# Optimization experiments

Hardware: AMD Instinct MI355X
Metric: run time of the kernel (lower is better)

The kernel has to match this reference:

```python
import jax, jax.numpy as jnp
import numpy as np

B, T, C, HS = 1024, 256, 384, 64

def setup_inputs() -> dict:
    key = jax.random.key(0)
    kx, kq, kk, kv = jax.random.split(key, 4)
    x = jax.random.normal(kx, (B, T, C), dtype=jnp.float32)
    # torch Linear(no bias): y = x @ W.T with W [hs, C]; store transposed [C, hs]
    s = 1.0 / np.sqrt(C)
    Wq = jax.random.uniform(kq, (C, HS), jnp.float32, -s, s)
    Wk = jax.random.uniform(kk, (C, HS), jnp.float32, -s, s)
    Wv = jax.random.uniform(kv, (C, HS), jnp.float32, -s, s)
    return {"x": x, "Wq": Wq, "Wk": Wk, "Wv": Wv}

def reference(x, Wq, Wk, Wv):
    Tn = x.shape[1]
    hs = Wq.shape[1]
    q = x @ Wq  # [B,T,hs]
    k = x @ Wk
    v = x @ Wv
    scores = jnp.einsum('bqd,bkd->bqk', q, k) * (hs ** -0.5)  # [B,T,T]
    causal = jnp.tril(jnp.ones((Tn, Tn), dtype=bool))
    scores = jnp.where(causal[None, :, :], scores, -jnp.inf)
    wei = jax.nn.softmax(scores, axis=-1)
    out = jnp.einsum('bqk,bkd->bqd', wei, v)  # [B,T,hs]
    return out
```

## Files before the change

### kernel.cpp

```cpp
#include <hip/hip_runtime.h>
#include <hip/hip_bf16.h>

#define TT 256
#define CC 384
#define HSZ 64

typedef __attribute__((ext_vector_type(8))) short bf16x8;
typedef __attribute__((ext_vector_type(4))) float f32x4;

static __device__ __forceinline__ unsigned short f2bf(float f) {
    union { __hip_bfloat16 h; unsigned short u; } cv;
    cv.h = __float2bfloat16(f);
    return cv.u;
}

static __device__ __forceinline__ bf16x8 cvt8(float4 a, float4 b) {
    bf16x8 r;
    r[0] = (short)f2bf(a.x); r[1] = (short)f2bf(a.y);
    r[2] = (short)f2bf(a.z); r[3] = (short)f2bf(a.w);
    r[4] = (short)f2bf(b.x); r[5] = (short)f2bf(b.y);
    r[6] = (short)f2bf(b.z); r[7] = (short)f2bf(b.w);
    return r;
}

__global__ __launch_bounds__(256) void wtrans_kernel(
        const float* __restrict__ Wq,
        const float* __restrict__ Wk,
        const float* __restrict__ Wv,
        unsigned short* __restrict__ Wt) {
    int idx = blockIdx.x * 256 + threadIdx.x;
    if (idx >= 192 * CC) return;
    int n = idx / CC;
    int ck = idx - n * CC;
    const float* W = (n < 64) ? Wq : ((n < 128) ? Wk : Wv);
    Wt[n * CC + ck] = f2bf(W[ck * HSZ + (n & 63)]);
}

__global__ __launch_bounds__(256, 2) void qkv_kernel(
        const float* __restrict__ x,
        const unsigned short* __restrict__ Wt,
        unsigned short* __restrict__ qw,
        unsigned short* __restrict__ kw,
        unsigned short* __restrict__ vtw) {
    const int lane = threadIdx.x & 63;
    const int wv   = threadIdx.x >> 6;
    const int c    = lane & 15;
    const int quad = lane >> 4;
    const int rowbase = blockIdx.x * 128 + wv * 32;

    f32x4 acc[2][12];
    #pragma unroll
    for (int t = 0; t < 2; ++t)
        #pragma unroll
        for (int n = 0; n < 12; ++n)
            acc[t][n] = (f32x4){0.f, 0.f, 0.f, 0.f};

    const float* xa0 = x + (size_t)(rowbase + c) * CC + quad * 8;
    const float* xa1 = xa0 + 16 * CC;
    const unsigned short* wb = Wt + c * CC + quad * 8;

    for (int s = 0; s < 12; ++s) {
        float4 a0lo = *(const float4*)(xa0 + s * 32);
        float4 a0hi = *(const float4*)(xa0 + s * 32 + 4);
        float4 a1lo = *(const float4*)(xa1 + s * 32);
        float4 a1hi = *(const float4*)(xa1 + s * 32 + 4);
        bf16x8 a0 = cvt8(a0lo, a0hi);
        bf16x8 a1 = cvt8(a1lo, a1hi);
        #pragma unroll
        for (int n = 0; n < 12; ++n) {
            bf16x8 b = *(const bf16x8*)(wb + n * 16 * CC + s * 32);
            acc[0][n] = __builtin_amdgcn_mfma_f32_16x16x32_bf16(a0, b, acc[0][n], 0, 0, 0);
            acc[1][n] = __builtin_amdgcn_mfma_f32_16x16x32_bf16(a1, b, acc[1][n], 0, 0, 0);
        }
    }

    #pragma unroll
    for (int t = 0; t < 2; ++t) {
        const int mbase = rowbase + t * 16 + quad * 4;
        #pragma unroll
        for (int n = 0; n < 8; ++n) {
            unsigned short* dst = (n < 4) ? qw : kw;
            const int cg = (n & 3) * 16 + c;
            #pragma unroll
            for (int r = 0; r < 4; ++r)
                dst[(size_t)(mbase + r) * HSZ + cg] = f2bf(acc[t][n][r]);
        }
        const int bidx = mbase >> 8;
        const int tok  = mbase & 255;
        #pragma unroll
        for (int n = 8; n < 12; ++n) {
            const int hsg = (n - 8) * 16 + c;
            ushort4 pk;
            pk.x = f2bf(acc[t][n][0]);
            pk.y = f2bf(acc[t][n][1]);
            pk.z = f2bf(acc[t][n][2]);
            pk.w = f2bf(acc[t][n][3]);
            *(ushort4*)(vtw + (size_t)bidx * (HSZ * TT) + hsg * TT + tok) = pk;
        }
    }
}

__global__ __launch_bounds__(256, 2) void attn_kernel(
        const unsigned short* __restrict__ qw,
        const unsigned short* __restrict__ kw,
        const unsigned short* __restrict__ vtw,
        float* __restrict__ outp) {
    __shared__ __align__(16) unsigned short pbuf[4][16][40];
    const int b    = blockIdx.x;
    const int lane = threadIdx.x & 63;
    const int wv   = threadIdx.x >> 6;
    const int c    = lane & 15;
    const int quad = lane >> 4;

    const unsigned short* qb = qw  + (size_t)b * TT * HSZ;
    const unsigned short* kb = kw  + (size_t)b * TT * HSZ;
    const unsigned short* vb = vtw + (size_t)b * HSZ * TT;
    float*                ob = outp + (size_t)b * TT * HSZ;

    bf16x8 qf[4][2];
    #pragma unroll
    for (int i = 0; i < 4; ++i) {
        const int rb = (wv + 4 * i) * 16;
        #pragma unroll
        for (int ks = 0; ks < 2; ++ks)
            qf[i][ks] = *(const bf16x8*)(qb + (rb + c) * HSZ + ks * 32 + quad * 8);
    }

    f32x4 of[4][4];
    f32x4 mst[4], lst[4];
    #pragma unroll
    for (int i = 0; i < 4; ++i) {
        mst[i] = (f32x4){-1e30f, -1e30f, -1e30f, -1e30f};
        lst[i] = (f32x4){0.f, 0.f, 0.f, 0.f};
        #pragma unroll
        for (int n = 0; n < 4; ++n)
            of[i][n] = (f32x4){0.f, 0.f, 0.f, 0.f};
    }

    const float qscale = 0.18033688011112042f;

    for (int kt = 0; kt < 8; ++kt) {
        const int k0 = kt * 32;
        bf16x8 kf[2][2], vf[4];
        #pragma unroll
        for (int nt = 0; nt < 2; ++nt)
            #pragma unroll
            for (int ks = 0; ks < 2; ++ks)
                kf[nt][ks] = *(const bf16x8*)(kb + (k0 + nt * 16 + c) * HSZ + ks * 32 + quad * 8);
        #pragma unroll
        for (int n = 0; n < 4; ++n)
            vf[n] = *(const bf16x8*)(vb + (n * 16 + c) * TT + k0 + quad * 8);

        #pragma unroll
        for (int i = 0; i < 4; ++i) {
            const int mt = wv + 4 * i;
            if (mt < 2 * kt) continue;
            const int rb = mt * 16;

            f32x4 s0 = {0.f, 0.f, 0.f, 0.f}, s1 = {0.f, 0.f, 0.f, 0.f};
            #pragma unroll
            for (int ks = 0; ks < 2; ++ks) {
                s0 = __builtin_amdgcn_mfma_f32_16x16x32_bf16(qf[i][ks], kf[0][ks], s0, 0, 0, 0);
                s1 = __builtin_amdgcn_mfma_f32_16x16x32_bf16(qf[i][ks], kf[1][ks], s1, 0, 0, 0);
            }

            f32x4 t0, t1;
            #pragma unroll
            for (int r = 0; r < 4; ++r) { t0[r] = s0[r] * qscale; t1[r] = s1[r] * qscale; }

            if (mt < 2 * kt + 2) {
                #pragma unroll
                for (int r = 0; r < 4; ++r) {
                    const int row = rb + quad * 4 + r;
                    if (k0 + c > row)      t0[r] = -1e30f;
                    if (k0 + 16 + c > row) t1[r] = -1e30f;
                }
            }

            f32x4 mx;
            #pragma unroll
            for (int r = 0; r < 4; ++r) mx[r] = fmaxf(t0[r], t1[r]);
            #pragma unroll
            for (int off = 1; off < 16; off <<= 1)
                #pragma unroll
                for (int r = 0; r < 4; ++r)
                    mx[r] = fmaxf(mx[r], __shfl_xor(mx[r], off, 64));

            f32x4 mnew, alpha, p0, p1, rs;
            #pragma unroll
            for (int r = 0; r < 4; ++r) {
                mnew[r]  = fmaxf(mst[i][r], mx[r]);
                alpha[r] = exp2f(mst[i][r] - mnew[r]);
                p0[r]    = exp2f(t0[r] - mnew[r]);
                p1[r]    = exp2f(t1[r] - mnew[r]);
                rs[r]    = p0[r] + p1[r];
                mst[i][r] = mnew[r];
            }
            #pragma unroll
            for (int off = 1; off < 16; off <<= 1)
                #pragma unroll
                for (int r = 0; r < 4; ++r)
                    rs[r] += __shfl_xor(rs[r], off, 64);
            #pragma unroll
            for (int r = 0; r < 4; ++r)
                lst[i][r] = lst[i][r] * alpha[r] + rs[r];

            #pragma unroll
            for (int n = 0; n < 4; ++n)
                #pragma unroll
                for (int r = 0; r < 4; ++r)
                    of[i][n][r] *= alpha[r];

            #pragma unroll
            for (int r = 0; r < 4; ++r) {
                pbuf[wv][quad * 4 + r][c]      = f2bf(p0[r]);
                pbuf[wv][quad * 4 + r][16 + c] = f2bf(p1[r]);
            }
            bf16x8 pf = *(const bf16x8*)(&pbuf[wv][c][quad * 8]);
            #pragma unroll
            for (int n = 0; n < 4; ++n)
                of[i][n] = __builtin_amdgcn_mfma_f32_16x16x32_bf16(pf, vf[n], of[i][n], 0, 0, 0);
        }
    }

    #pragma unroll
    for (int i = 0; i < 4; ++i) {
        const int rb = (wv + 4 * i) * 16;
        f32x4 inv;
        #pragma unroll
        for (int r = 0; r < 4; ++r) inv[r] = 1.f / lst[i][r];
        #pragma unroll
        for (int n = 0; n < 4; ++n)
            #pragma unroll
            for (int r = 0; r < 4; ++r)
                ob[(size_t)(rb + quad * 4 + r) * HSZ + n * 16 + c] = of[i][n][r] * inv[r];
    }
}

extern "C" void kernel_launch(void* const* d_in, const int* in_sizes, int n_in,
                              void* d_out, int out_size, void* d_ws, size_t ws_size,
                              hipStream_t stream) {
    const float* x  = (const float*)d_in[0];
    const float* Wq = (const float*)d_in[1];
    const float* Wk = (const float*)d_in[2];
    const float* Wv = (const float*)d_in[3];
    float* outp = (float*)d_out;

    const int Bn = in_sizes[0] / (TT * CC);
    const size_t QKV_BYTES = (size_t)Bn * TT * HSZ * 2;

    char* ws = (char*)d_ws;
    unsigned short* Wt  = (unsigned short*)ws;
    unsigned short* qw  = (unsigned short*)(ws + (1u << 18));
    unsigned short* kw  = (unsigned short*)(ws + (1u << 18) + QKV_BYTES);
    unsigned short* vtw = (unsigned short*)(ws + (1u << 18) + 2 * QKV_BYTES);

    hipLaunchKernelGGL(wtrans_kernel, dim3(288), dim3(256), 0, stream, Wq, Wk, Wv, Wt);
    hipLaunchKernelGGL(qkv_kernel, dim3(Bn * 2), dim3(256), 0, stream, x, Wt, qw, kw, vtw);
    hipLaunchKernelGGL(attn_kernel, dim3(Bn), dim3(256), 0, stream, qw, kw, vtw, outp);
}
```

Baseline: 704.8 us.

## Fuse QKV projection and causal attention into one kernel with LDS-resident K/V

```diff
diff --git a/kernel.cpp b/kernel.cpp
--- a/kernel.cpp
+++ b/kernel.cpp
@@ -36,17 +36,22 @@
     Wt[n * CC + ck] = f2bf(W[ck * HSZ + (n & 63)]);
 }
 
-__global__ __launch_bounds__(256, 2) void qkv_kernel(
+__global__ __launch_bounds__(512, 2) void fused_kernel(
         const float* __restrict__ x,
         const unsigned short* __restrict__ Wt,
-        unsigned short* __restrict__ qw,
-        unsigned short* __restrict__ kw,
-        unsigned short* __restrict__ vtw) {
+        float* __restrict__ outp) {
+    __shared__ __align__(16) unsigned short k_lds[TT][72];
+    __shared__ __align__(16) unsigned short v_lds[HSZ][264];
+    __shared__ __align__(16) unsigned short pbuf[8][16][40];
+
+    const int b    = blockIdx.x;
     const int lane = threadIdx.x & 63;
-    const int wv   = threadIdx.x >> 6;
+    const int w    = threadIdx.x >> 6;
     const int c    = lane & 15;
     const int quad = lane >> 4;
-    const int rowbase = blockIdx.x * 128 + wv * 32;
+
+    const int Rl0 = 16 * w;
+    const int Rl1 = 240 - 16 * w;
 
     f32x4 acc[2][12];
     #pragma unroll
@@ -55,8 +60,8 @@
         for (int n = 0; n < 12; ++n)
             acc[t][n] = (f32x4){0.f, 0.f, 0.f, 0.f};
 
-    const float* xa0 = x + (size_t)(rowbase + c) * CC + quad * 8;
-    const float* xa1 = xa0 + 16 * CC;
+    const float* xa0 = x + ((size_t)b * TT + Rl0 + c) * CC + quad * 8;
+    const float* xa1 = x + ((size_t)b * TT + Rl1 + c) * CC + quad * 8;
     const unsigned short* wb = Wt + c * CC + quad * 8;
 
     for (int s = 0; s < 12; ++s) {
@@ -68,25 +73,23 @@
         bf16x8 a1 = cvt8(a1lo, a1hi);
         #pragma unroll
         for (int n = 0; n < 12; ++n) {
-            bf16x8 b = *(const bf16x8*)(wb + n * 16 * CC + s * 32);
-            acc[0][n] = __builtin_amdgcn_mfma_f32_16x16x32_bf16(a0, b, acc[0][n], 0, 0, 0);
-            acc[1][n] = __builtin_amdgcn_mfma_f32_16x16x32_bf16(a1, b, acc[1][n], 0, 0, 0);
-        }
-    }
-
+            bf16x8 bf = *(const bf16x8*)(wb + n * 16 * CC + s * 32);
+            acc[0][n] = __builtin_amdgcn_mfma_f32_16x16x32_bf16(a0, bf, acc[0][n], 0, 0, 0);
+            acc[1][n] = __builtin_amdgcn_mfma_f32_16x16x32_bf16(a1, bf, acc[1][n], 0, 0, 0);
+        }
+    }
+
+    bf16x8 qf[2][2];
     #pragma unroll
     for (int t = 0; t < 2; ++t) {
-        const int mbase = rowbase + t * 16 + quad * 4;
-        #pragma unroll
-        for (int n = 0; n < 8; ++n) {
-            unsigned short* dst = (n < 4) ? qw : kw;
-            const int cg = (n & 3) * 16 + c;
+        const int lr = (t == 0 ? Rl0 : Rl1) + quad * 4;
+        #pragma unroll
+        for (int n = 4; n < 8; ++n) {
+            const int cg = (n - 4) * 16 + c;
             #pragma unroll
             for (int r = 0; r < 4; ++r)
-                dst[(size_t)(mbase + r) * HSZ + cg] = f2bf(acc[t][n][r]);
-        }
-        const int bidx = mbase >> 8;
-        const int tok  = mbase & 255;
+                k_lds[lr + r][cg] = f2bf(acc[t][n][r]);
+        }
         #pragma unroll
         for (int n = 8; n < 12; ++n) {
             const int hsg = (n - 8) * 16 + c;
@@ -95,41 +98,30 @@
             pk.y = f2bf(acc[t][n][1]);
             pk.z = f2bf(acc[t][n][2]);
             pk.w = f2bf(acc[t][n][3]);
-            *(ushort4*)(vtw + (size_t)bidx * (HSZ * TT) + hsg * TT + tok) = pk;
-        }
-    }
-}
-
-__global__ __launch_bounds__(256, 2) void attn_kernel(
-        const unsigned short* __restrict__ qw,
-        const unsigned short* __restrict__ kw,
-        const unsigned short* __restrict__ vtw,
-        float* __restrict__ outp) {
-    __shared__ __align__(16) unsigned short pbuf[4][16][40];
-    const int b    = blockIdx.x;
-    const int lane = threadIdx.x & 63;
-    const int wv   = threadIdx.x >> 6;
-    const int c    = lane & 15;
-    const int quad = lane >> 4;
-
-    const unsigned short* qb = qw  + (size_t)b * TT * HSZ;
-    const unsigned short* kb = kw  + (size_t)b * TT * HSZ;
-    const unsigned short* vb = vtw + (size_t)b * HSZ * TT;
-    float*                ob = outp + (size_t)b * TT * HSZ;
-
-    bf16x8 qf[4][2];
-    #pragma unroll
-    for (int i = 0; i < 4; ++i) {
-        const int rb = (wv + 4 * i) * 16;
-        #pragma unroll
-        for (int ks = 0; ks < 2; ++ks)
-            qf[i][ks] = *(const bf16x8*)(qb + (rb + c) * HSZ + ks * 32 + quad * 8);
-    }
-
-    f32x4 of[4][4];
-    f32x4 mst[4], lst[4];
-    #pragma unroll
-    for (int i = 0; i < 4; ++i) {
+            *(ushort4*)(&v_lds[hsg][lr]) = pk;
+        }
+        #pragma unroll
+        for (int p = 0; p < 2; ++p) {
+            #pragma unroll
+            for (int n2 = 0; n2 < 2; ++n2) {
+                const int n = 2 * p + n2;
+                #pragma unroll
+                for (int r = 0; r < 4; ++r)
+                    pbuf[w][quad * 4 + r][n2 * 16 + c] = f2bf(acc[t][n][r]);
+            }
+            qf[t][p] = *(const bf16x8*)(&pbuf[w][c][quad * 8]);
+        }
+    }
+
+    __syncthreads();
+
+    const int mt0 = w;
+    const int mt1 = 15 - w;
+
+    f32x4 of[2][4];
+    f32x4 mst[2], lst[2];
+    #pragma unroll
+    for (int i = 0; i < 2; ++i) {
         mst[i] = (f32x4){-1e30f, -1e30f, -1e30f, -1e30f};
         lst[i] = (f32x4){0.f, 0.f, 0.f, 0.f};
         #pragma unroll
@@ -140,28 +132,30 @@
     const float qscale = 0.18033688011112042f;
 
     for (int kt = 0; kt < 8; ++kt) {
+        if (mt1 < 2 * kt) break;
         const int k0 = kt * 32;
+
         bf16x8 kf[2][2], vf[4];
         #pragma unroll
         for (int nt = 0; nt < 2; ++nt)
             #pragma unroll
             for (int ks = 0; ks < 2; ++ks)
-                kf[nt][ks] = *(const bf16x8*)(kb + (k0 + nt * 16 + c) * HSZ + ks * 32 + quad * 8);
+                kf[nt][ks] = *(const bf16x8*)(&k_lds[k0 + nt * 16 + c][ks * 32 + quad * 8]);
         #pragma unroll
         for (int n = 0; n < 4; ++n)
-            vf[n] = *(const bf16x8*)(vb + (n * 16 + c) * TT + k0 + quad * 8);
-
-        #pragma unroll
-        for (int i = 0; i < 4; ++i) {
-            const int mt = wv + 4 * i;
+            vf[n] = *(const bf16x8*)(&v_lds[n * 16 + c][k0 + quad * 8]);
+
+        #pragma unroll
+        for (int ti = 0; ti < 2; ++ti) {
+            const int mt = (ti == 0) ? mt0 : mt1;
             if (mt < 2 * kt) continue;
             const int rb = mt * 16;
 
             f32x4 s0 = {0.f, 0.f, 0.f, 0.f}, s1 = {0.f, 0.f, 0.f, 0.f};
             #pragma unroll
             for (int ks = 0; ks < 2; ++ks) {
-                s0 = __builtin_amdgcn_mfma_f32_16x16x32_bf16(qf[i][ks], kf[0][ks], s0, 0, 0, 0);
-                s1 = __builtin_amdgcn_mfma_f32_16x16x32_bf16(qf[i][ks], kf[1][ks], s1, 0, 0, 0);
+                s0 = __builtin_amdgcn_mfma_f32_16x16x32_bf16(qf[ti][ks], kf[0][ks], s0, 0, 0, 0);
+                s1 = __builtin_amdgcn_mfma_f32_16x16x32_bf16(qf[ti][ks], kf[1][ks], s1, 0, 0, 0);
             }
 
             f32x4 t0, t1;
@@ -189,12 +183,12 @@
             f32x4 mnew, alpha, p0, p1, rs;
             #pragma unroll
             for (int r = 0; r < 4; ++r) {
-                mnew[r]  = fmaxf(mst[i][r], mx[r]);
-                alpha[r] = exp2f(mst[i][r] - mnew[r]);
+                mnew[r]  = fmaxf(mst[ti][r], mx[r]);
+                alpha[r] = exp2f(mst[ti][r] - mnew[r]);
                 p0[r]    = exp2f(t0[r] - mnew[r]);
                 p1[r]    = exp2f(t1[r] - mnew[r]);
                 rs[r]    = p0[r] + p1[r];
-                mst[i][r] = mnew[r];
+                mst[ti][r] = mnew[r];
             }
             #pragma unroll
             for (int off = 1; off < 16; off <<= 1)
@@ -203,37 +197,38 @@
                     rs[r] += __shfl_xor(rs[r], off, 64);
             #pragma unroll
             for (int r = 0; r < 4; ++r)
-                lst[i][r] = lst[i][r] * alpha[r] + rs[r];
+                lst[ti][r] = lst[ti][r] * alpha[r] + rs[r];
 
             #pragma unroll
             for (int n = 0; n < 4; ++n)
                 #pragma unroll
                 for (int r = 0; r < 4; ++r)
-                    of[i][n][r] *= alpha[r];
+                    of[ti][n][r] *= alpha[r];
 
             #pragma unroll
             for (int r = 0; r < 4; ++r) {
-                pbuf[wv][quad * 4 + r][c]      = f2bf(p0[r]);
-                pbuf[wv][quad * 4 + r][16 + c] = f2bf(p1[r]);
-            }
-            bf16x8 pf = *(const bf16x8*)(&pbuf[wv][c][quad * 8]);
+                pbuf[w][quad * 4 + r][c]      = f2bf(p0[r]);
+                pbuf[w][quad * 4 + r][16 + c] = f2bf(p1[r]);
+            }
+            bf16x8 pf = *(const bf16x8*)(&pbuf[w][c][quad * 8]);
             #pragma unroll
             for (int n = 0; n < 4; ++n)
-                of[i][n] = __builtin_amdgcn_mfma_f32_16x16x32_bf16(pf, vf[n], of[i][n], 0, 0, 0);
-        }
-    }
-
-    #pragma unroll
-    for (int i = 0; i < 4; ++i) {
-        const int rb = (wv + 4 * i) * 16;
+                of[ti][n] = __builtin_amdgcn_mfma_f32_16x16x32_bf16(pf, vf[n], of[ti][n], 0, 0, 0);
+        }
+    }
+
+    float* ob = outp + (size_t)b * TT * HSZ;
+    #pragma unroll
+    for (int ti = 0; ti < 2; ++ti) {
+        const int rb = ((ti == 0) ? mt0 : mt1) * 16;
         f32x4 inv;
         #pragma unroll
-        for (int r = 0; r < 4; ++r) inv[r] = 1.f / lst[i][r];
+        for (int r = 0; r < 4; ++r) inv[r] = 1.f / lst[ti][r];
         #pragma unroll
         for (int n = 0; n < 4; ++n)
             #pragma unroll
             for (int r = 0; r < 4; ++r)
-                ob[(size_t)(rb + quad * 4 + r) * HSZ + n * 16 + c] = of[i][n][r] * inv[r];
+                ob[(size_t)(rb + quad * 4 + r) * HSZ + n * 16 + c] = of[ti][n][r] * inv[r];
     }
 }
 
@@ -247,15 +242,9 @@
     float* outp = (float*)d_out;
 
     const int Bn = in_sizes[0] / (TT * CC);
-    const size_t QKV_BYTES = (size_t)Bn * TT * HSZ * 2;
-
-    char* ws = (char*)d_ws;
-    unsigned short* Wt  = (unsigned short*)ws;
-    unsigned short* qw  = (unsigned short*)(ws + (1u << 18));
-    unsigned short* kw  = (unsigned short*)(ws + (1u << 18) + QKV_BYTES);
-    unsigned short* vtw = (unsigned short*)(ws + (1u << 18) + 2 * QKV_BYTES);
+
+    unsigned short* Wt = (unsigned short*)d_ws;
 
     hipLaunchKernelGGL(wtrans_kernel, dim3(288), dim3(256), 0, stream, Wq, Wk, Wv, Wt);
-    hipLaunchKernelGGL(qkv_kernel, dim3(Bn * 2), dim3(256), 0, stream, x, Wt, qw, kw, vtw);
-    hipLaunchKernelGGL(attn_kernel, dim3(Bn), dim3(256), 0, stream, qw, kw, vtw, outp);
-}
+    hipLaunchKernelGGL(fused_kernel, dim3(Bn), dim3(512), 0, stream, x, Wt, outp);
+}
```

After: 660.3 us. 1.07x faster.
